# Optimization experiments

Measured on AMD Instinct MI355X. Metric: run time of the kernel, lower is better.

Reference implementation:

```python
import jax, jax.numpy as jnp
import numpy as np

B, LC, LQ, D, F = 16, 2048, 256, 768, 768
MASK_VALUE = -1.0e12


def setup_inputs() -> dict:
    key = jax.random.key(0)
    ks = jax.random.split(key, 6)
    scale = 1.0 / np.sqrt(D)
    return {
        "x_cont": jax.random.normal(ks[0], (B, LC, D), dtype=jnp.float32),
        "x_ques": jax.random.normal(ks[1], (B, LQ, D), dtype=jnp.float32),
        "ques_len": jax.random.randint(ks[2], (B, 1), 0, LQ, dtype=jnp.int32),
        "WC": jax.random.normal(ks[3], (D, F), dtype=jnp.float32) * scale,
        "WQ": jax.random.normal(ks[4], (D, F), dtype=jnp.float32) * scale,
        "V": jax.random.normal(ks[5], (2 * D, F), dtype=jnp.float32) * scale,
    }


def _mask_logits(logits, ques_len):
    # Original: one_hot(ques_len[:,0], Lq) -> 1 - cumsum along Lq -> tile over Lc.
    # mask[b, j] = 1 if j < ques_len[b] else 0.
    lq = logits.shape[-1]
    oh = jax.nn.one_hot(ques_len[:, 0], lq, dtype=jnp.float32)  # [B, Lq]
    valid = 1.0 - jnp.cumsum(oh, axis=1)                         # [B, Lq]
    return logits + MASK_VALUE * (1.0 - valid)[:, None, :]       # broadcast over Lc


def reference(x_cont, x_ques, ques_len, WC, WQ, V):
    filters = WC.shape[-1]
    x_cont_ = jax.nn.relu(jnp.einsum("bcd,df->bcf", x_cont, WC))  # [B, Lc, F]
    x_ques_ = jax.nn.relu(jnp.einsum("bqd,df->bqf", x_ques, WQ))  # [B, Lq, F]
    logits = jnp.einsum("bcf,bqf->bcq", x_cont_, x_ques_) / jnp.sqrt(
        jnp.asarray(filters, dtype=x_cont.dtype)
    )  # [B, Lc, Lq]
    logits = _mask_logits(logits, ques_len)
    attn = jax.nn.softmax(logits, axis=-1)
    C = jnp.einsum("bcq,bqd->bcd", attn, x_ques)                  # [B, Lc, D]
    res = jnp.concatenate([x_cont, C], axis=2)                    # [B, Lc, 2D]
    gate = jax.nn.sigmoid(jnp.einsum("bce,ef->bcf", res, V))      # [B, Lc, F]
    return gate
```

## Files before the change

### kernel.cpp

```cpp
#include <hip/hip_runtime.h>
#include <hip/hip_bf16.h>
#include <cstdint>


using bf16 = __hip_bfloat16;
typedef __attribute__((ext_vector_type(8))) __bf16 bf16x8;
typedef __attribute__((ext_vector_type(4))) float f32x4;

typedef __attribute__((address_space(1))) const uint32_t GU32;
typedef __attribute__((address_space(3))) uint32_t LU32;

__device__ __forceinline__ void gll16(const bf16* g, bf16* l) {
  __builtin_amdgcn_global_load_lds((GU32*)g, (LU32*)l, 16, 0, 0);
}
__device__ __forceinline__ f32x4 mfma_bf16(bf16x8 a, bf16x8 b, f32x4 c) {
  return __builtin_amdgcn_mfma_f32_16x16x32_bf16(a, b, c, 0, 0, 0);
}
__device__ __forceinline__ bf16x8 ld_frag(const bf16* p) {
  return *reinterpret_cast<const bf16x8*>(p);
}
__device__ __forceinline__ int swz(int r) { return (r & 3) ^ ((r >> 2) & 1); }

__device__ __forceinline__ unsigned short f2bf_bits(float x) {
  bf16 b = __float2bfloat16(x);
  union { bf16 b; unsigned short s; } u;
  u.b = b;
  return u.s;
}

__global__ void transpose_f32_bf16(const float* __restrict__ in, bf16* __restrict__ out,
                                   int R, int C) {
  __shared__ float tile[32][33];
  int c0 = blockIdx.x * 32, r0 = blockIdx.y * 32;
  int tx = threadIdx.x, ty = threadIdx.y;
#pragma unroll
  for (int i = ty; i < 32; i += 8)
    tile[i][tx] = in[(long)(r0 + i) * C + (c0 + tx)];
  __syncthreads();
#pragma unroll
  for (int i = ty; i < 32; i += 8)
    out[(long)(c0 + i) * R + (r0 + tx)] = __float2bfloat16(tile[tx][i]);
}

__global__ void transpose_bf16(const bf16* __restrict__ in, bf16* __restrict__ out,
                               int R, int C, long ibs, long obs) {
  __shared__ bf16 tile[32][33];
  const bf16* inb = in + (long)blockIdx.z * ibs;
  bf16* outb = out + (long)blockIdx.z * obs;
  int c0 = blockIdx.x * 32, r0 = blockIdx.y * 32;
  int tx = threadIdx.x, ty = threadIdx.y;
#pragma unroll
  for (int i = ty; i < 32; i += 8)
    tile[i][tx] = inb[(long)(r0 + i) * C + (c0 + tx)];
  __syncthreads();
#pragma unroll
  for (int i = ty; i < 32; i += 8)
    outb[(long)(c0 + i) * R + (r0 + tx)] = tile[tx][i];
}

__global__ void convert_flat(const float* __restrict__ in, bf16* __restrict__ out, long n4) {
  long i = (long)blockIdx.x * blockDim.x + threadIdx.x;
  if (i >= n4) return;
  float4 v = reinterpret_cast<const float4*>(in)[i];
  ushort4 o;
  o.x = f2bf_bits(v.x);
  o.y = f2bf_bits(v.y);
  o.z = f2bf_bits(v.z);
  o.w = f2bf_bits(v.w);
  reinterpret_cast<ushort4*>(out)[i] = o;
}

__global__ __launch_bounds__(256) void gemm_bt_split(
    const bf16* __restrict__ A, long lda,
    const bf16* __restrict__ Bt, long ldb,
    bf16* __restrict__ O1, bf16* __restrict__ O2, int K) {
  __shared__ __align__(16) bf16 As[128 * 32];
  __shared__ __align__(16) bf16 Bs[128 * 32];
  const int tid = threadIdx.x;
  const int wave = tid >> 6;
  const int lane = tid & 63;
  const int l16 = lane & 15;
  const int kh = lane >> 4;
  const int wm = (wave >> 1) * 64;
  const int wn = (wave & 1) * 64;
  const long row0 = (long)blockIdx.x * 128;
  const long col0 = (long)blockIdx.y * 128;
  const int srow = tid >> 2;
  const int scol = ((tid & 3) ^ swz(srow)) * 8;

  const bf16* ap0 = A + (row0 + srow) * lda + scol;
  const bf16* ap1 = ap0 + 64 * lda;
  const bf16* bp0 = Bt + (col0 + srow) * ldb + scol;
  const bf16* bp1 = bp0 + 64 * ldb;
  bf16* as0 = As + wave * 512;
  bf16* as1 = as0 + 2048;
  bf16* bs0 = Bs + wave * 512;
  bf16* bs1 = bs0 + 2048;

  const int xc = (kh ^ swz(l16)) * 8;
  f32x4 acc[4][4] = {};

  for (int k0 = 0; k0 < K; k0 += 32) {
    gll16(ap0 + k0, as0);
    gll16(ap1 + k0, as1);
    gll16(bp0 + k0, bs0);
    gll16(bp1 + k0, bs1);
    __syncthreads();
    bf16x8 af[4], bfr[4];
#pragma unroll
    for (int i = 0; i < 4; ++i)
      af[i] = ld_frag(As + (wm + i * 16 + l16) * 32 + xc);
#pragma unroll
    for (int j = 0; j < 4; ++j)
      bfr[j] = ld_frag(Bs + (wn + j * 16 + l16) * 32 + xc);
#pragma unroll
    for (int i = 0; i < 4; ++i)
#pragma unroll
      for (int j = 0; j < 4; ++j)
        acc[i][j] = mfma_bf16(af[i], bfr[j], acc[i][j]);
    __syncthreads();
  }

  const bool isO1 = col0 < 768;
#pragma unroll
  for (int i = 0; i < 4; ++i)
#pragma unroll
    for (int j = 0; j < 4; ++j)
#pragma unroll
      for (int r = 0; r < 4; ++r) {
        long row = row0 + wm + i * 16 + kh * 4 + r;
        long col = col0 + wn + j * 16 + l16;
        float v = acc[i][j][r];
        if (isO1)
          O1[row * 768 + col] = __float2bfloat16(fmaxf(v, 0.0f));
        else
          O2[row * 768 + (col - 768)] = __float2bfloat16(v);
      }
}

__global__ __launch_bounds__(512, 2) void gemm4b(
    const bf16* __restrict__ A, long lda,
    const bf16* __restrict__ Bt, long ldb,
    bf16* __restrict__ O1, bf16* __restrict__ O2, int K) {
  extern __shared__ __align__(16) bf16 smem[];
  const int tid = threadIdx.x;
  const int wid = tid >> 6;
  const int lane = tid & 63;
  const int l15 = lane & 15;
  const int g = lane >> 4;
  const int wm = wid >> 2;
  const int wn = wid & 3;

  const int lin = blockIdx.x;
  const int per = (int)gridDim.x >> 3;
  const int wgid = (lin & 7) * per + (lin >> 3);
  const long row0 = (long)(wgid / 6) * 256;
  const long col0 = (long)(wgid % 6) * 256;

  const int srow = lane >> 2;
  const int sc = ((lane & 3) ^ swz(srow)) * 8;
  const int w16 = wid * 16;
  const bf16* Ab = A + (row0 + srow) * lda + sc;
  const bf16* Bb = Bt + (col0 + srow) * ldb + sc;

  f32x4 acc[8][4] = {};

  auto stageA = [&](int buf, int kk) {
    bf16* d = smem + buf * 16384 + w16 * 32;
    gll16(Ab + (long)w16 * lda + kk, d);
    gll16(Ab + (long)(128 + w16) * lda + kk, d + 128 * 32);
  };
  auto stageB = [&](int buf, int kk) {
    bf16* d = smem + buf * 16384 + 8192 + w16 * 32;
    gll16(Bb + (long)w16 * ldb + kk, d);
    gll16(Bb + (long)(128 + w16) * ldb + kk, d + 128 * 32);
  };
  const int xc = (g ^ swz(l15)) * 8;
  auto ldA = [&](int buf, int m) {
    int row = wm * 128 + m * 16 + l15;
    return ld_frag(smem + buf * 16384 + row * 32 + xc);
  };
  auto ldB = [&](int buf, int n) {
    int row = wn * 64 + n * 16 + l15;
    return ld_frag(smem + buf * 16384 + 8192 + row * 32 + xc);
  };

  stageA(0, 0);
  stageB(0, 0);
  stageA(1, 32);
  stageB(1, 32);
  stageA(2, 64);
  stageB(2, 64);
  asm volatile("s_waitcnt vmcnt(8)\n\ts_barrier" ::: "memory");

  const int NT = K >> 5;
  bf16x8 av[4], bv[4];

  for (int t = 0; t < NT; ++t) {
    const int cur = t & 3;
    const int pfb = (t + 3) & 3;
    const bool pf = (t + 3) < NT;
    const int kk = (t + 3) << 5;

#pragma unroll
    for (int n = 0; n < 4; ++n) bv[n] = ldB(cur, n);
#pragma unroll
    for (int m = 0; m < 4; ++m) av[m] = ldA(cur, m);
    if (pf) stageA(pfb, kk);
    __builtin_amdgcn_s_barrier();
    __builtin_amdgcn_s_setprio(1);
#pragma unroll
    for (int m = 0; m < 4; ++m)
#pragma unroll
      for (int n = 0; n < 4; ++n) acc[m][n] = mfma_bf16(av[m], bv[n], acc[m][n]);
    __builtin_amdgcn_s_setprio(0);
    __builtin_amdgcn_s_barrier();

#pragma unroll
    for (int m = 0; m < 4; ++m) av[m] = ldA(cur, 4 + m);
    if (pf) stageB(pfb, kk);
    __builtin_amdgcn_s_barrier();
    __builtin_amdgcn_s_setprio(1);
#pragma unroll
    for (int m = 0; m < 4; ++m)
#pragma unroll
      for (int n = 0; n < 4; ++n)
        acc[4 + m][n] = mfma_bf16(av[m], bv[n], acc[4 + m][n]);
    __builtin_amdgcn_s_setprio(0);

    if (t <= NT - 4)
      asm volatile("s_waitcnt vmcnt(8)\n\ts_barrier" ::: "memory");
    else if (t == NT - 3)
      asm volatile("s_waitcnt vmcnt(4)\n\ts_barrier" ::: "memory");
    else if (t == NT - 2)
      asm volatile("s_waitcnt vmcnt(0)\n\ts_barrier" ::: "memory");
  }

  const bool isO1 = col0 < 768;
#pragma unroll
  for (int m = 0; m < 8; ++m)
#pragma unroll
    for (int n = 0; n < 4; ++n)
#pragma unroll
      for (int r = 0; r < 4; ++r) {
        long row = row0 + wm * 128 + m * 16 + g * 4 + r;
        long col = col0 + wn * 64 + n * 16 + l15;
        float v = acc[m][n][r];
        if (isO1)
          O1[row * 768 + col] = __float2bfloat16(fmaxf(v, 0.0f));
        else
          O2[row * 768 + (col - 768)] = __float2bfloat16(v);
      }
}

__global__ __launch_bounds__(512, 2) void attn_kernel(
    const bf16* __restrict__ xcW, const bf16* __restrict__ xqW,
    const bf16* __restrict__ xqVT, const bf16* __restrict__ G1,
    const int* __restrict__ qlen_arr, float* __restrict__ out) {
  extern __shared__ __align__(16) bf16 smem[];
  bf16* P = smem + 24576;
  float* wred = (float*)(smem + 58368);
  float* wsum = wred + 512;

  const int n = blockIdx.x;
  const int xcd = n & 7;
  const int idx = n >> 3;
  const int b = xcd * 2 + (idx >> 4);
  const int ct = idx & 15;

  const int tid = threadIdx.x;
  const int wid = tid >> 6;
  const int lane = tid & 63;
  const int l16 = lane & 15;
  const int kh = lane >> 4;
  const int wr = wid >> 2;
  const int wc = wid & 3;

  const long crow0 = (long)b * 2048 + (long)ct * 128;
  const int srow = lane >> 2;
  const int sc = ((lane & 3) ^ swz(srow)) * 8;
  const int xcr = (kh ^ swz(l16)) * 8;

  const bf16* ap = xcW + (crow0 + wid * 16 + srow) * 768 + sc;
  const bf16* bp = xqW + ((long)b * 256 + wid * 32 + srow) * 768 + sc;
  const bf16* bp2 = bp + 16 * 768;

  auto stage = [&](int bufi, int k0) {
    gll16(ap + k0, smem + bufi * 4096 + wid * 512);
    gll16(bp + k0, smem + 8192 + bufi * 8192 + wid * 1024);
    gll16(bp2 + k0, smem + 8192 + bufi * 8192 + wid * 1024 + 512);
  };

  f32x4 acc[4][4] = {};
  stage(0, 0);

  for (int t = 0; t < 24; ++t) {
    const int cur = t & 1;
    if (t + 1 < 24) {
      stage(cur ^ 1, (t + 1) * 32);
      asm volatile("s_waitcnt vmcnt(3)\n\ts_barrier" ::: "memory");
    } else {
      asm volatile("s_waitcnt vmcnt(0)\n\ts_barrier" ::: "memory");
    }
    const bf16* Ac = smem + cur * 4096;
    const bf16* Bc = smem + 8192 + cur * 8192;
    bf16x8 af[4], bfr[4];
#pragma unroll
    for (int i = 0; i < 4; ++i)
      af[i] = ld_frag(Ac + (wr * 64 + i * 16 + l16) * 32 + xcr);
#pragma unroll
    for (int j = 0; j < 4; ++j)
      bfr[j] = ld_frag(Bc + (wc * 64 + j * 16 + l16) * 32 + xcr);
    __builtin_amdgcn_s_setprio(1);
#pragma unroll
    for (int i = 0; i < 4; ++i)
#pragma unroll
      for (int j = 0; j < 4; ++j)
        acc[i][j] = mfma_bf16(af[i], bfr[j], acc[i][j]);
    __builtin_amdgcn_s_setprio(0);
    __builtin_amdgcn_s_barrier();
  }

  const float scale = 0.036084391824351615f;
  const int qlen = qlen_arr[b];

#pragma unroll
  for (int i = 0; i < 4; ++i)
#pragma unroll
    for (int j = 0; j < 4; ++j) {
      int col = wc * 64 + j * 16 + l16;
      float m = (col >= qlen) ? -1.0e12f : 0.0f;
#pragma unroll
      for (int r = 0; r < 4; ++r)
        acc[i][j][r] = acc[i][j][r] * scale + m;
    }

#pragma unroll
  for (int i = 0; i < 4; ++i)
#pragma unroll
    for (int r = 0; r < 4; ++r) {
      float mx = fmaxf(fmaxf(acc[i][0][r], acc[i][1][r]),
                       fmaxf(acc[i][2][r], acc[i][3][r]));
      mx = fmaxf(mx, __shfl_xor(mx, 1));
      mx = fmaxf(mx, __shfl_xor(mx, 2));
      mx = fmaxf(mx, __shfl_xor(mx, 4));
      mx = fmaxf(mx, __shfl_xor(mx, 8));
      if (l16 == 0) wred[(wr * 64 + i * 16 + kh * 4 + r) * 4 + wc] = mx;
    }
  __syncthreads();

#pragma unroll
  for (int i = 0; i < 4; ++i)
#pragma unroll
    for (int r = 0; r < 4; ++r) {
      int row = wr * 64 + i * 16 + kh * 4 + r;
      float gm = fmaxf(fmaxf(wred[row * 4 + 0], wred[row * 4 + 1]),
                       fmaxf(wred[row * 4 + 2], wred[row * 4 + 3]));
      float s = 0.0f;
#pragma unroll
      for (int j = 0; j < 4; ++j) {
        float e = expf(acc[i][j][r] - gm);
        acc[i][j][r] = e;
        s += e;
      }
      s += __shfl_xor(s, 1);
      s += __shfl_xor(s, 2);
      s += __shfl_xor(s, 4);
      s += __shfl_xor(s, 8);
      if (l16 == 0) wsum[row * 4 + wc] = s;
    }
  __syncthreads();

#pragma unroll
  for (int i = 0; i < 4; ++i)
#pragma unroll
    for (int r = 0; r < 4; ++r) {
      int row = wr * 64 + i * 16 + kh * 4 + r;
      float inv = 1.0f / (wsum[row * 4 + 0] + wsum[row * 4 + 1] +
                          wsum[row * 4 + 2] + wsum[row * 4 + 3]);
#pragma unroll
      for (int j = 0; j < 4; ++j)
        P[row * 264 + wc * 64 + j * 16 + l16] = __float2bfloat16(acc[i][j][r] * inv);
    }
  __syncthreads();

  bf16x8 pf[4][8];
#pragma unroll
  for (int i = 0; i < 4; ++i)
#pragma unroll
    for (int kk = 0; kk < 8; ++kk)
      pf[i][kk] = ld_frag(P + (wr * 64 + i * 16 + l16) * 264 + kk * 32 + kh * 8);

  for (int nb = 0; nb < 3; ++nb) {
    const int n0 = nb * 256 + wc * 64;
    const bf16* btp = xqVT + ((long)b * 768 + n0) * 256;
    f32x4 a2[4][4] = {};
#pragma unroll
    for (int kk = 0; kk < 8; ++kk) {
      bf16x8 vf[4];
#pragma unroll
      for (int j = 0; j < 4; ++j)
        vf[j] = ld_frag(btp + (j * 16 + l16) * 256 + kk * 32 + kh * 8);
#pragma unroll
      for (int i = 0; i < 4; ++i)
#pragma unroll
        for (int j = 0; j < 4; ++j)
          a2[i][j] = mfma_bf16(pf[i][kk], vf[j], a2[i][j]);
    }
#pragma unroll
    for (int i = 0; i < 4; ++i)
#pragma unroll
      for (int j = 0; j < 4; ++j)
#pragma unroll
        for (int r = 0; r < 4; ++r) {
          long row = crow0 + wr * 64 + i * 16 + kh * 4 + r;
          int col = n0 + j * 16 + l16;
          float v = a2[i][j][r] + __bfloat162float(G1[row * 768 + col]);
          out[row * 768 + col] = 1.0f / (1.0f + __expf(-v));
        }
  }
}

extern "C" void kernel_launch(void* const* d_in, const int* in_sizes, int n_in,
                              void* d_out, int out_size, void* d_ws, size_t ws_size,
                              hipStream_t stream) {
  const float* x_cont = (const float*)d_in[0];
  const float* x_ques = (const float*)d_in[1];
  const int* ques_len = (const int*)d_in[2];
  const float* WC = (const float*)d_in[3];
  const float* WQ = (const float*)d_in[4];
  const float* V = (const float*)d_in[5];
  float* out = (float*)d_out;

  bf16* Wct = (bf16*)d_ws;
  bf16* Wqt = Wct + (long)1536 * 768;
  bf16* xcB = Wqt + (long)1536 * 768;
  bf16* xqB = xcB + (long)32768 * 768;
  bf16* xcW = xqB + (long)4096 * 768;
  bf16* xqW = xcW + (long)32768 * 768;
  bf16* xqV = xqW + (long)4096 * 768;
  bf16* xqVT = xqV + (long)4096 * 768;
  bf16* G1 = xqVT + (long)16 * 768 * 256;

  (void)hipFuncSetAttribute(reinterpret_cast<const void*>(&gemm4b),
                            hipFuncAttributeMaxDynamicSharedMemorySize, 131072);
  (void)hipFuncSetAttribute(reinterpret_cast<const void*>(&attn_kernel),
                            hipFuncAttributeMaxDynamicSharedMemorySize, 131072);

  transpose_f32_bf16<<<dim3(24, 24), dim3(32, 8), 0, stream>>>(WC, Wct, 768, 768);
  transpose_f32_bf16<<<dim3(24, 24), dim3(32, 8), 0, stream>>>(
      V, Wct + (long)768 * 768, 768, 768);
  transpose_f32_bf16<<<dim3(24, 24), dim3(32, 8), 0, stream>>>(WQ, Wqt, 768, 768);
  transpose_f32_bf16<<<dim3(24, 24), dim3(32, 8), 0, stream>>>(
      V + (long)768 * 768, Wqt + (long)768 * 768, 768, 768);

  convert_flat<<<24576, 256, 0, stream>>>(x_cont, xcB, (long)32768 * 768 / 4);
  convert_flat<<<3072, 256, 0, stream>>>(x_ques, xqB, (long)4096 * 768 / 4);

  gemm_bt_split<<<dim3(32, 12), 256, 0, stream>>>(xqB, 768, Wqt, 768, xqW, xqV, 768);
  transpose_bf16<<<dim3(24, 8, 16), dim3(32, 8), 0, stream>>>(
      xqV, xqVT, 256, 768, (long)256 * 768, (long)768 * 256);

  gemm4b<<<768, 512, 131072, stream>>>(xcB, 768, Wct, 768, xcW, G1, 768);

  attn_kernel<<<256, 512, 120832, stream>>>(xcW, xqW, xqVT, G1, ques_len, out);
}
```

Measured before the change: 255.7 us.

## Skip masked question columns in attention and merge weight transposes

The attention kernel now uses 64-row context tiles with 4 waves, each owning a 64-column slice of the question axis. Waves whose slice lies entirely beyond the question length skip loading and computing logits, and the P·V loop stops after the last valid 32-wide k step. The four weight transposes are merged into one launch over blockIdx.z. This saves work proportional to the masked fraction, in exchange for more blocks, per-wave divergence and some lost reuse of A tiles.

```diff
diff --git a/kernel.cpp b/kernel.cpp
--- a/kernel.cpp
+++ b/kernel.cpp
@@ -28,18 +28,23 @@
   return u.s;
 }
 
-__global__ void transpose_f32_bf16(const float* __restrict__ in, bf16* __restrict__ out,
-                                   int R, int C) {
+__global__ void transpose4(const float* __restrict__ s0, const float* __restrict__ s1,
+                           const float* __restrict__ s2, const float* __restrict__ s3,
+                           bf16* __restrict__ d0, bf16* __restrict__ d1,
+                           bf16* __restrict__ d2, bf16* __restrict__ d3) {
   __shared__ float tile[32][33];
+  const int z = blockIdx.z;
+  const float* in = (z == 0) ? s0 : (z == 1) ? s1 : (z == 2) ? s2 : s3;
+  bf16* out = (z == 0) ? d0 : (z == 1) ? d1 : (z == 2) ? d2 : d3;
   int c0 = blockIdx.x * 32, r0 = blockIdx.y * 32;
   int tx = threadIdx.x, ty = threadIdx.y;
 #pragma unroll
   for (int i = ty; i < 32; i += 8)
-    tile[i][tx] = in[(long)(r0 + i) * C + (c0 + tx)];
+    tile[i][tx] = in[(long)(r0 + i) * 768 + (c0 + tx)];
   __syncthreads();
 #pragma unroll
   for (int i = ty; i < 32; i += 8)
-    out[(long)(c0 + i) * R + (r0 + tx)] = __float2bfloat16(tile[tx][i]);
+    out[(long)(c0 + i) * 768 + (r0 + tx)] = __float2bfloat16(tile[tx][i]);
 }
 
 __global__ void transpose_bf16(const bf16* __restrict__ in, bf16* __restrict__ out,
@@ -253,42 +258,46 @@
       }
 }
 
-__global__ __launch_bounds__(512, 2) void attn_kernel(
+__global__ __launch_bounds__(256) void attn_kernel(
     const bf16* __restrict__ xcW, const bf16* __restrict__ xqW,
     const bf16* __restrict__ xqVT, const bf16* __restrict__ G1,
     const int* __restrict__ qlen_arr, float* __restrict__ out) {
   extern __shared__ __align__(16) bf16 smem[];
-  bf16* P = smem + 24576;
-  float* wred = (float*)(smem + 58368);
-  float* wsum = wred + 512;
+  bf16* P = smem + 20480;
+  float* wred = (float*)(smem + 37376);
+  float* wsum = wred + 256;
 
   const int n = blockIdx.x;
-  const int xcd = n & 7;
-  const int idx = n >> 3;
-  const int b = xcd * 2 + (idx >> 4);
-  const int ct = idx & 15;
+  const int b = n & 15;
+  const int ct = n >> 4;
 
   const int tid = threadIdx.x;
-  const int wid = tid >> 6;
+  const int wc = tid >> 6;
   const int lane = tid & 63;
   const int l16 = lane & 15;
   const int kh = lane >> 4;
-  const int wr = wid >> 2;
-  const int wc = wid & 3;
-
-  const long crow0 = (long)b * 2048 + (long)ct * 128;
+
+  const int qlen = qlen_arr[b];
+  const int qeff = (qlen == 0) ? 256 : qlen;
+  const bool active = (wc * 64) < qeff;
+  const int kkmax = (qeff + 31) >> 5;
+
+  const long crow0 = (long)b * 2048 + (long)ct * 64;
   const int srow = lane >> 2;
   const int sc = ((lane & 3) ^ swz(srow)) * 8;
   const int xcr = (kh ^ swz(l16)) * 8;
 
-  const bf16* ap = xcW + (crow0 + wid * 16 + srow) * 768 + sc;
-  const bf16* bp = xqW + ((long)b * 256 + wid * 32 + srow) * 768 + sc;
-  const bf16* bp2 = bp + 16 * 768;
+  const bf16* ap = xcW + (crow0 + wc * 16 + srow) * 768 + sc;
+  const bf16* bp = xqW + ((long)b * 256 + wc * 64 + srow) * 768 + sc;
 
   auto stage = [&](int bufi, int k0) {
-    gll16(ap + k0, smem + bufi * 4096 + wid * 512);
-    gll16(bp + k0, smem + 8192 + bufi * 8192 + wid * 1024);
-    gll16(bp2 + k0, smem + 8192 + bufi * 8192 + wid * 1024 + 512);
+    gll16(ap + k0, smem + bufi * 2048 + wc * 512);
+    if (active) {
+      bf16* bd = smem + 4096 + bufi * 8192 + wc * 2048;
+#pragma unroll
+      for (int q = 0; q < 4; ++q)
+        gll16(bp + q * 16 * 768 + k0, bd + q * 512);
+    }
   };
 
   f32x4 acc[4][4] = {};
@@ -298,98 +307,122 @@
     const int cur = t & 1;
     if (t + 1 < 24) {
       stage(cur ^ 1, (t + 1) * 32);
-      asm volatile("s_waitcnt vmcnt(3)\n\ts_barrier" ::: "memory");
+      if (active)
+        asm volatile("s_waitcnt vmcnt(5)" ::: "memory");
+      else
+        asm volatile("s_waitcnt vmcnt(1)" ::: "memory");
+      __builtin_amdgcn_s_barrier();
     } else {
       asm volatile("s_waitcnt vmcnt(0)\n\ts_barrier" ::: "memory");
     }
-    const bf16* Ac = smem + cur * 4096;
-    const bf16* Bc = smem + 8192 + cur * 8192;
-    bf16x8 af[4], bfr[4];
-#pragma unroll
-    for (int i = 0; i < 4; ++i)
-      af[i] = ld_frag(Ac + (wr * 64 + i * 16 + l16) * 32 + xcr);
-#pragma unroll
-    for (int j = 0; j < 4; ++j)
-      bfr[j] = ld_frag(Bc + (wc * 64 + j * 16 + l16) * 32 + xcr);
-    __builtin_amdgcn_s_setprio(1);
-#pragma unroll
-    for (int i = 0; i < 4; ++i)
+    if (active) {
+      const bf16* Ac = smem + cur * 2048;
+      const bf16* Bc = smem + 4096 + cur * 8192;
+      bf16x8 af[4], bfr[4];
+#pragma unroll
+      for (int i = 0; i < 4; ++i)
+        af[i] = ld_frag(Ac + (i * 16 + l16) * 32 + xcr);
 #pragma unroll
       for (int j = 0; j < 4; ++j)
-        acc[i][j] = mfma_bf16(af[i], bfr[j], acc[i][j]);
-    __builtin_amdgcn_s_setprio(0);
+        bfr[j] = ld_frag(Bc + (wc * 64 + j * 16 + l16) * 32 + xcr);
+      __builtin_amdgcn_s_setprio(1);
+#pragma unroll
+      for (int i = 0; i < 4; ++i)
+#pragma unroll
+        for (int j = 0; j < 4; ++j)
+          acc[i][j] = mfma_bf16(af[i], bfr[j], acc[i][j]);
+      __builtin_amdgcn_s_setprio(0);
+    }
     __builtin_amdgcn_s_barrier();
   }
 
   const float scale = 0.036084391824351615f;
-  const int qlen = qlen_arr[b];
-
-#pragma unroll
-  for (int i = 0; i < 4; ++i)
-#pragma unroll
-    for (int j = 0; j < 4; ++j) {
-      int col = wc * 64 + j * 16 + l16;
-      float m = (col >= qlen) ? -1.0e12f : 0.0f;
+
+  if (active) {
+#pragma unroll
+    for (int i = 0; i < 4; ++i)
+#pragma unroll
+      for (int j = 0; j < 4; ++j) {
+        int col = wc * 64 + j * 16 + l16;
+        float m = (col >= qeff) ? -1.0e12f : 0.0f;
+#pragma unroll
+        for (int r = 0; r < 4; ++r)
+          acc[i][j][r] = acc[i][j][r] * scale + m;
+      }
+#pragma unroll
+    for (int i = 0; i < 4; ++i)
+#pragma unroll
+      for (int r = 0; r < 4; ++r) {
+        float mx = fmaxf(fmaxf(acc[i][0][r], acc[i][1][r]),
+                         fmaxf(acc[i][2][r], acc[i][3][r]));
+        mx = fmaxf(mx, __shfl_xor(mx, 1));
+        mx = fmaxf(mx, __shfl_xor(mx, 2));
+        mx = fmaxf(mx, __shfl_xor(mx, 4));
+        mx = fmaxf(mx, __shfl_xor(mx, 8));
+        if (l16 == 0) wred[(i * 16 + kh * 4 + r) * 4 + wc] = mx;
+      }
+  } else if (l16 == 0) {
+#pragma unroll
+    for (int i = 0; i < 4; ++i)
 #pragma unroll
       for (int r = 0; r < 4; ++r)
-        acc[i][j][r] = acc[i][j][r] * scale + m;
-    }
-
-#pragma unroll
-  for (int i = 0; i < 4; ++i)
-#pragma unroll
-    for (int r = 0; r < 4; ++r) {
-      float mx = fmaxf(fmaxf(acc[i][0][r], acc[i][1][r]),
-                       fmaxf(acc[i][2][r], acc[i][3][r]));
-      mx = fmaxf(mx, __shfl_xor(mx, 1));
-      mx = fmaxf(mx, __shfl_xor(mx, 2));
-      mx = fmaxf(mx, __shfl_xor(mx, 4));
-      mx = fmaxf(mx, __shfl_xor(mx, 8));
-      if (l16 == 0) wred[(wr * 64 + i * 16 + kh * 4 + r) * 4 + wc] = mx;
-    }
+        wred[(i * 16 + kh * 4 + r) * 4 + wc] = -3.0e38f;
+  }
   __syncthreads();
 
-#pragma unroll
-  for (int i = 0; i < 4; ++i)
-#pragma unroll
-    for (int r = 0; r < 4; ++r) {
-      int row = wr * 64 + i * 16 + kh * 4 + r;
-      float gm = fmaxf(fmaxf(wred[row * 4 + 0], wred[row * 4 + 1]),
-                       fmaxf(wred[row * 4 + 2], wred[row * 4 + 3]));
-      float s = 0.0f;
-#pragma unroll
-      for (int j = 0; j < 4; ++j) {
-        float e = expf(acc[i][j][r] - gm);
-        acc[i][j][r] = e;
-        s += e;
-      }
-      s += __shfl_xor(s, 1);
-      s += __shfl_xor(s, 2);
-      s += __shfl_xor(s, 4);
-      s += __shfl_xor(s, 8);
-      if (l16 == 0) wsum[row * 4 + wc] = s;
-    }
+  if (active) {
+#pragma unroll
+    for (int i = 0; i < 4; ++i)
+#pragma unroll
+      for (int r = 0; r < 4; ++r) {
+        int row = i * 16 + kh * 4 + r;
+        float gm = fmaxf(fmaxf(wred[row * 4 + 0], wred[row * 4 + 1]),
+                         fmaxf(wred[row * 4 + 2], wred[row * 4 + 3]));
+        float s = 0.0f;
+#pragma unroll
+        for (int j = 0; j < 4; ++j) {
+          float e = expf(acc[i][j][r] - gm);
+          acc[i][j][r] = e;
+          s += e;
+        }
+        s += __shfl_xor(s, 1);
+        s += __shfl_xor(s, 2);
+        s += __shfl_xor(s, 4);
+        s += __shfl_xor(s, 8);
+        if (l16 == 0) wsum[row * 4 + wc] = s;
+      }
+  } else if (l16 == 0) {
+#pragma unroll
+    for (int i = 0; i < 4; ++i)
+#pragma unroll
+      for (int r = 0; r < 4; ++r)
+        wsum[(i * 16 + kh * 4 + r) * 4 + wc] = 0.0f;
+  }
   __syncthreads();
 
-#pragma unroll
-  for (int i = 0; i < 4; ++i)
-#pragma unroll
-    for (int r = 0; r < 4; ++r) {
-      int row = wr * 64 + i * 16 + kh * 4 + r;
-      float inv = 1.0f / (wsum[row * 4 + 0] + wsum[row * 4 + 1] +
-                          wsum[row * 4 + 2] + wsum[row * 4 + 3]);
-#pragma unroll
-      for (int j = 0; j < 4; ++j)
-        P[row * 264 + wc * 64 + j * 16 + l16] = __float2bfloat16(acc[i][j][r] * inv);
-    }
+  if (active) {
+#pragma unroll
+    for (int i = 0; i < 4; ++i)
+#pragma unroll
+      for (int r = 0; r < 4; ++r) {
+        int row = i * 16 + kh * 4 + r;
+        float inv = 1.0f / (wsum[row * 4 + 0] + wsum[row * 4 + 1] +
+                            wsum[row * 4 + 2] + wsum[row * 4 + 3]);
+#pragma unroll
+        for (int j = 0; j < 4; ++j)
+          P[row * 264 + wc * 64 + j * 16 + l16] = __float2bfloat16(acc[i][j][r] * inv);
+      }
+  }
   __syncthreads();
 
   bf16x8 pf[4][8];
 #pragma unroll
-  for (int i = 0; i < 4; ++i)
-#pragma unroll
-    for (int kk = 0; kk < 8; ++kk)
-      pf[i][kk] = ld_frag(P + (wr * 64 + i * 16 + l16) * 264 + kk * 32 + kh * 8);
+  for (int kk = 0; kk < 8; ++kk) {
+    if (kk >= kkmax) break;
+#pragma unroll
+    for (int i = 0; i < 4; ++i)
+      pf[i][kk] = ld_frag(P + (i * 16 + l16) * 264 + kk * 32 + kh * 8);
+  }
 
   for (int nb = 0; nb < 3; ++nb) {
     const int n0 = nb * 256 + wc * 64;
@@ -397,6 +430,7 @@
     f32x4 a2[4][4] = {};
 #pragma unroll
     for (int kk = 0; kk < 8; ++kk) {
+      if (kk >= kkmax) break;
       bf16x8 vf[4];
 #pragma unroll
       for (int j = 0; j < 4; ++j)
@@ -413,7 +447,7 @@
       for (int j = 0; j < 4; ++j)
 #pragma unroll
         for (int r = 0; r < 4; ++r) {
-          long row = crow0 + wr * 64 + i * 16 + kh * 4 + r;
+          long row = crow0 + i * 16 + kh * 4 + r;
           int col = n0 + j * 16 + l16;
           float v = a2[i][j][r] + __bfloat162float(G1[row * 768 + col]);
           out[row * 768 + col] = 1.0f / (1.0f + __expf(-v));
@@ -445,14 +479,11 @@
   (void)hipFuncSetAttribute(reinterpret_cast<const void*>(&gemm4b),
                             hipFuncAttributeMaxDynamicSharedMemorySize, 131072);
   (void)hipFuncSetAttribute(reinterpret_cast<const void*>(&attn_kernel),
-                            hipFuncAttributeMaxDynamicSharedMemorySize, 131072);
-
-  transpose_f32_bf16<<<dim3(24, 24), dim3(32, 8), 0, stream>>>(WC, Wct, 768, 768);
-  transpose_f32_bf16<<<dim3(24, 24), dim3(32, 8), 0, stream>>>(
-      V, Wct + (long)768 * 768, 768, 768);
-  transpose_f32_bf16<<<dim3(24, 24), dim3(32, 8), 0, stream>>>(WQ, Wqt, 768, 768);
-  transpose_f32_bf16<<<dim3(24, 24), dim3(32, 8), 0, stream>>>(
-      V + (long)768 * 768, Wqt + (long)768 * 768, 768, 768);
+                            hipFuncAttributeMaxDynamicSharedMemorySize, 76800);
+
+  transpose4<<<dim3(24, 24, 4), dim3(32, 8), 0, stream>>>(
+      WC, WQ, V, V + (long)768 * 768,
+      Wct, Wqt, Wct + (long)768 * 768, Wqt + (long)768 * 768);
 
   convert_flat<<<24576, 256, 0, stream>>>(x_cont, xcB, (long)32768 * 768 / 4);
   convert_flat<<<3072, 256, 0, stream>>>(x_ques, xqB, (long)4096 * 768 / 4);
@@ -463,5 +494,5 @@
 
   gemm4b<<<768, 512, 131072, stream>>>(xcB, 768, Wct, 768, xcW, G1, 768);
 
-  attn_kernel<<<256, 512, 120832, stream>>>(xcW, xqW, xqVT, G1, ques_len, out);
-}
+  attn_kernel<<<512, 256, 76800, stream>>>(xcW, xqW, xqVT, G1, ques_len, out);
+}
```

New measurement: 264.9 us. 1.04x slower.

## Deepen attention QK pipeline to 4-stage ring and merge weight transposes

Applied to the files above, without the earlier changes.

The attention kernel's QK^T loop moves from a double-buffered load scheme to a 4-buffer ring that keeps three stages of global-to-LDS loads in flight, with vmcnt waits adjusted for each tail iteration. The P/softmax scratch now overlays the staging buffers, which shrinks dynamic LDS from 120832 to 102400 bytes. The four weight-transpose launches are merged into one launch that uses blockIdx.z to pick the matrix, cutting launch overhead. The deeper prefetch is meant to hide global latency in the 24-step K loop, at the cost of more LDS per block and the launch bound dropping its min-blocks hint.

```diff
diff --git a/kernel.cpp b/kernel.cpp
--- a/kernel.cpp
+++ b/kernel.cpp
@@ -28,18 +28,23 @@
   return u.s;
 }
 
-__global__ void transpose_f32_bf16(const float* __restrict__ in, bf16* __restrict__ out,
-                                   int R, int C) {
+__global__ void transpose4(const float* __restrict__ s0, const float* __restrict__ s1,
+                           const float* __restrict__ s2, const float* __restrict__ s3,
+                           bf16* __restrict__ d0, bf16* __restrict__ d1,
+                           bf16* __restrict__ d2, bf16* __restrict__ d3) {
   __shared__ float tile[32][33];
+  const int z = blockIdx.z;
+  const float* in = (z == 0) ? s0 : (z == 1) ? s1 : (z == 2) ? s2 : s3;
+  bf16* out = (z == 0) ? d0 : (z == 1) ? d1 : (z == 2) ? d2 : d3;
   int c0 = blockIdx.x * 32, r0 = blockIdx.y * 32;
   int tx = threadIdx.x, ty = threadIdx.y;
 #pragma unroll
   for (int i = ty; i < 32; i += 8)
-    tile[i][tx] = in[(long)(r0 + i) * C + (c0 + tx)];
+    tile[i][tx] = in[(long)(r0 + i) * 768 + (c0 + tx)];
   __syncthreads();
 #pragma unroll
   for (int i = ty; i < 32; i += 8)
-    out[(long)(c0 + i) * R + (r0 + tx)] = __float2bfloat16(tile[tx][i]);
+    out[(long)(c0 + i) * 768 + (r0 + tx)] = __float2bfloat16(tile[tx][i]);
 }
 
 __global__ void transpose_bf16(const bf16* __restrict__ in, bf16* __restrict__ out,
@@ -253,28 +258,28 @@
       }
 }
 
-__global__ __launch_bounds__(512, 2) void attn_kernel(
+__global__ __launch_bounds__(512) void attn3(
     const bf16* __restrict__ xcW, const bf16* __restrict__ xqW,
     const bf16* __restrict__ xqVT, const bf16* __restrict__ G1,
     const int* __restrict__ qlen_arr, float* __restrict__ out) {
   extern __shared__ __align__(16) bf16 smem[];
-  bf16* P = smem + 24576;
-  float* wred = (float*)(smem + 58368);
+  bf16* P = smem;
+  float* wred = (float*)(smem + 49152);
   float* wsum = wred + 512;
 
-  const int n = blockIdx.x;
-  const int xcd = n & 7;
-  const int idx = n >> 3;
-  const int b = xcd * 2 + (idx >> 4);
-  const int ct = idx & 15;
+  const int lin = blockIdx.x;
+  const int xcd = lin & 7;
+  const int jj = lin >> 3;
+  const int b = xcd * 2 + (jj >> 4);
+  const int ct = jj & 15;
 
   const int tid = threadIdx.x;
   const int wid = tid >> 6;
   const int lane = tid & 63;
   const int l16 = lane & 15;
   const int kh = lane >> 4;
-  const int wr = wid >> 2;
-  const int wc = wid & 3;
+  const int wm = wid >> 2;
+  const int wn = wid & 3;
 
   const long crow0 = (long)b * 2048 + (long)ct * 128;
   const int srow = lane >> 2;
@@ -285,32 +290,39 @@
   const bf16* bp = xqW + ((long)b * 256 + wid * 32 + srow) * 768 + sc;
   const bf16* bp2 = bp + 16 * 768;
 
-  auto stage = [&](int bufi, int k0) {
-    gll16(ap + k0, smem + bufi * 4096 + wid * 512);
-    gll16(bp + k0, smem + 8192 + bufi * 8192 + wid * 1024);
-    gll16(bp2 + k0, smem + 8192 + bufi * 8192 + wid * 1024 + 512);
+  auto stage = [&](int buf, int k0) {
+    gll16(ap + k0, smem + buf * 12288 + wid * 512);
+    bf16* bd = smem + buf * 12288 + 4096 + wid * 1024;
+    gll16(bp + k0, bd);
+    gll16(bp2 + k0, bd + 512);
   };
 
   f32x4 acc[4][4] = {};
   stage(0, 0);
+  stage(1, 32);
+  stage(2, 64);
 
   for (int t = 0; t < 24; ++t) {
-    const int cur = t & 1;
-    if (t + 1 < 24) {
-      stage(cur ^ 1, (t + 1) * 32);
+    const int cur = t & 3;
+    if (t + 3 < 24) stage((t + 3) & 3, (t + 3) * 32);
+    if (t <= 20)
+      asm volatile("s_waitcnt vmcnt(9)\n\ts_barrier" ::: "memory");
+    else if (t == 21)
+      asm volatile("s_waitcnt vmcnt(6)\n\ts_barrier" ::: "memory");
+    else if (t == 22)
       asm volatile("s_waitcnt vmcnt(3)\n\ts_barrier" ::: "memory");
-    } else {
+    else
       asm volatile("s_waitcnt vmcnt(0)\n\ts_barrier" ::: "memory");
-    }
-    const bf16* Ac = smem + cur * 4096;
-    const bf16* Bc = smem + 8192 + cur * 8192;
+
+    const bf16* Ac = smem + cur * 12288;
+    const bf16* Bc = Ac + 4096;
     bf16x8 af[4], bfr[4];
 #pragma unroll
     for (int i = 0; i < 4; ++i)
-      af[i] = ld_frag(Ac + (wr * 64 + i * 16 + l16) * 32 + xcr);
+      af[i] = ld_frag(Ac + (wm * 64 + i * 16 + l16) * 32 + xcr);
 #pragma unroll
     for (int j = 0; j < 4; ++j)
-      bfr[j] = ld_frag(Bc + (wc * 64 + j * 16 + l16) * 32 + xcr);
+      bfr[j] = ld_frag(Bc + (wn * 64 + j * 16 + l16) * 32 + xcr);
     __builtin_amdgcn_s_setprio(1);
 #pragma unroll
     for (int i = 0; i < 4; ++i)
@@ -328,7 +340,7 @@
   for (int i = 0; i < 4; ++i)
 #pragma unroll
     for (int j = 0; j < 4; ++j) {
-      int col = wc * 64 + j * 16 + l16;
+      int col = wn * 64 + j * 16 + l16;
       float m = (col >= qlen) ? -1.0e12f : 0.0f;
 #pragma unroll
       for (int r = 0; r < 4; ++r)
@@ -345,7 +357,7 @@
       mx = fmaxf(mx, __shfl_xor(mx, 2));
       mx = fmaxf(mx, __shfl_xor(mx, 4));
       mx = fmaxf(mx, __shfl_xor(mx, 8));
-      if (l16 == 0) wred[(wr * 64 + i * 16 + kh * 4 + r) * 4 + wc] = mx;
+      if (l16 == 0) wred[(wm * 64 + i * 16 + kh * 4 + r) * 4 + wn] = mx;
     }
   __syncthreads();
 
@@ -353,7 +365,7 @@
   for (int i = 0; i < 4; ++i)
 #pragma unroll
     for (int r = 0; r < 4; ++r) {
-      int row = wr * 64 + i * 16 + kh * 4 + r;
+      int row = wm * 64 + i * 16 + kh * 4 + r;
       float gm = fmaxf(fmaxf(wred[row * 4 + 0], wred[row * 4 + 1]),
                        fmaxf(wred[row * 4 + 2], wred[row * 4 + 3]));
       float s = 0.0f;
@@ -367,7 +379,7 @@
       s += __shfl_xor(s, 2);
       s += __shfl_xor(s, 4);
       s += __shfl_xor(s, 8);
-      if (l16 == 0) wsum[row * 4 + wc] = s;
+      if (l16 == 0) wsum[row * 4 + wn] = s;
     }
   __syncthreads();
 
@@ -375,12 +387,12 @@
   for (int i = 0; i < 4; ++i)
 #pragma unroll
     for (int r = 0; r < 4; ++r) {
-      int row = wr * 64 + i * 16 + kh * 4 + r;
+      int row = wm * 64 + i * 16 + kh * 4 + r;
       float inv = 1.0f / (wsum[row * 4 + 0] + wsum[row * 4 + 1] +
                           wsum[row * 4 + 2] + wsum[row * 4 + 3]);
 #pragma unroll
       for (int j = 0; j < 4; ++j)
-        P[row * 264 + wc * 64 + j * 16 + l16] = __float2bfloat16(acc[i][j][r] * inv);
+        P[row * 264 + wn * 64 + j * 16 + l16] = __float2bfloat16(acc[i][j][r] * inv);
     }
   __syncthreads();
 
@@ -389,10 +401,10 @@
   for (int i = 0; i < 4; ++i)
 #pragma unroll
     for (int kk = 0; kk < 8; ++kk)
-      pf[i][kk] = ld_frag(P + (wr * 64 + i * 16 + l16) * 264 + kk * 32 + kh * 8);
+      pf[i][kk] = ld_frag(P + (wm * 64 + i * 16 + l16) * 264 + kk * 32 + kh * 8);
 
   for (int nb = 0; nb < 3; ++nb) {
-    const int n0 = nb * 256 + wc * 64;
+    const int n0 = nb * 256 + wn * 64;
     const bf16* btp = xqVT + ((long)b * 768 + n0) * 256;
     f32x4 a2[4][4] = {};
 #pragma unroll
@@ -413,7 +425,7 @@
       for (int j = 0; j < 4; ++j)
 #pragma unroll
         for (int r = 0; r < 4; ++r) {
-          long row = crow0 + wr * 64 + i * 16 + kh * 4 + r;
+          long row = crow0 + wm * 64 + i * 16 + kh * 4 + r;
           int col = n0 + j * 16 + l16;
           float v = a2[i][j][r] + __bfloat162float(G1[row * 768 + col]);
           out[row * 768 + col] = 1.0f / (1.0f + __expf(-v));
@@ -444,15 +456,12 @@
 
   (void)hipFuncSetAttribute(reinterpret_cast<const void*>(&gemm4b),
                             hipFuncAttributeMaxDynamicSharedMemorySize, 131072);
-  (void)hipFuncSetAttribute(reinterpret_cast<const void*>(&attn_kernel),
-                            hipFuncAttributeMaxDynamicSharedMemorySize, 131072);
-
-  transpose_f32_bf16<<<dim3(24, 24), dim3(32, 8), 0, stream>>>(WC, Wct, 768, 768);
-  transpose_f32_bf16<<<dim3(24, 24), dim3(32, 8), 0, stream>>>(
-      V, Wct + (long)768 * 768, 768, 768);
-  transpose_f32_bf16<<<dim3(24, 24), dim3(32, 8), 0, stream>>>(WQ, Wqt, 768, 768);
-  transpose_f32_bf16<<<dim3(24, 24), dim3(32, 8), 0, stream>>>(
-      V + (long)768 * 768, Wqt + (long)768 * 768, 768, 768);
+  (void)hipFuncSetAttribute(reinterpret_cast<const void*>(&attn3),
+                            hipFuncAttributeMaxDynamicSharedMemorySize, 102400);
+
+  transpose4<<<dim3(24, 24, 4), dim3(32, 8), 0, stream>>>(
+      WC, WQ, V, V + (long)768 * 768,
+      Wct, Wqt, Wct + (long)768 * 768, Wqt + (long)768 * 768);
 
   convert_flat<<<24576, 256, 0, stream>>>(x_cont, xcB, (long)32768 * 768 / 4);
   convert_flat<<<3072, 256, 0, stream>>>(x_ques, xqB, (long)4096 * 768 / 4);
@@ -463,5 +472,5 @@
 
   gemm4b<<<768, 512, 131072, stream>>>(xcB, 768, Wct, 768, xcW, G1, 768);
 
-  attn_kernel<<<256, 512, 120832, stream>>>(xcW, xqW, xqVT, G1, ques_len, out);
-}
+  attn3<<<256, 512, 102400, stream>>>(xcW, xqW, xqVT, G1, ques_len, out);
+}
```

After: 248.1 us. 3.0% less time.
